# Performance work log

Hardware: AMD Instinct MI355X
Metric: run time of the kernel (lower is better)

The kernel has to match this reference:

```python
import jax, jax.numpy as jnp
import numpy as np

N_HEAD = 16
NEG = -1e9

def setup_inputs() -> dict:
    key = jax.random.key(0)
    k1, k2, k3 = jax.random.split(key, 3)
    B, S, NX = 8, 1024, 1024
    x = jax.random.normal(k1, (B, S, NX), dtype=jnp.float32)
    w_attn = jax.random.normal(k2, (NX, 3 * NX), dtype=jnp.float32) * 0.02
    b_attn = jnp.zeros((3 * NX,), dtype=jnp.float32)
    w_proj = jax.random.normal(k3, (NX, NX), dtype=jnp.float32) * 0.02
    b_proj = jnp.zeros((NX,), dtype=jnp.float32)
    return {"x": x, "w_attn": w_attn, "b_attn": b_attn, "w_proj": w_proj, "b_proj": b_proj}

def reference(x, w_attn, b_attn, w_proj, b_proj):
    B, S, NX = x.shape
    H = N_HEAD
    D = NX // H
    qkv = x @ w_attn + b_attn                      # [B,S,3*NX]
    q, k, v = jnp.split(qkv, 3, axis=-1)           # each [B,S,NX]
    q = q.reshape(B, S, H, D)
    k = k.reshape(B, S, H, D)
    v = v.reshape(B, S, H, D)
    # scores with scale (scale=True -> divide by sqrt(head_dim))
    w = jnp.einsum('bqhd,bkhd->bhqk', q, k) / jnp.sqrt(jnp.float32(D))
    tril = jnp.tril(jnp.ones((S, S), dtype=w.dtype))  # causal mask buffer
    w = w * tril + NEG * (1.0 - tril)
    w = jax.nn.softmax(w, axis=-1)                 # dropout is identity at eval
    a = jnp.einsum('bhqk,bkhd->bqhd', w, v)        # [B,S,H,D]
    a = a.reshape(B, S, NX)
    a = a @ w_proj + b_proj
    return a
```

## Files before the change

kernel.cpp:

```cpp
#include <hip/hip_runtime.h>
#include <hip/hip_bf16.h>
#include <stdint.h>

typedef __bf16 bf16x8 __attribute__((ext_vector_type(8)));
typedef float  f32x4  __attribute__((ext_vector_type(4)));
typedef float  f32x16 __attribute__((ext_vector_type(16)));

__device__ __forceinline__ void gload_lds16(const void* g, void* l) {
  __builtin_amdgcn_global_load_lds(
      (const __attribute__((address_space(1))) unsigned int*)g,
      (__attribute__((address_space(3))) unsigned int*)l, 16, 0, 0);
}

__global__ void k_cast(const float* __restrict__ in, __bf16* __restrict__ out, int n4) {
  int i = blockIdx.x * blockDim.x + threadIdx.x;
  if (i >= n4) return;
  float4 v = reinterpret_cast<const float4*>(in)[i];
  union { __bf16 h[4]; uint64_t u; } c;
  c.h[0] = (__bf16)v.x; c.h[1] = (__bf16)v.y; c.h[2] = (__bf16)v.z; c.h[3] = (__bf16)v.w;
  *reinterpret_cast<uint64_t*>(out + 4l * i) = c.u;
}

__global__ void k_transpose_cast(const float* __restrict__ in, __bf16* __restrict__ out,
                                 int R, int C) {
  __shared__ float t[32][33];
  const int tx = threadIdx.x & 31, ty = threadIdx.x >> 5;
  const int c0 = blockIdx.x * 32, r0 = blockIdx.y * 32;
#pragma unroll
  for (int rr = 0; rr < 4; ++rr)
    t[ty * 4 + rr][tx] = in[(long)(r0 + ty * 4 + rr) * C + c0 + tx];
  __syncthreads();
#pragma unroll
  for (int rr = 0; rr < 4; ++rr)
    out[(long)(c0 + ty * 4 + rr) * R + r0 + tx] = (__bf16)t[tx][ty * 4 + rr];
}

template <int MODE>
__global__ void k_gemm_bt(const __bf16* __restrict__ A, const __bf16* __restrict__ Bt,
                          const float* __restrict__ bias, int M, int N, int K,
                          __bf16* __restrict__ qo, __bf16* __restrict__ ko,
                          __bf16* __restrict__ vo, float* __restrict__ fo) {
  __shared__ __bf16 Ab[128 * 32];
  __shared__ __bf16 Bb[128 * 32];
  const int l = threadIdx.x & 63, w = threadIdx.x >> 6;
  const int wr = w >> 1, wc = w & 1;
  const int bm = blockIdx.y, bn = blockIdx.x;

  f32x4 acc[4][4] = {};

  const __bf16* Ag = A + (long)(bm * 128 + w * 32 + (l >> 2)) * K + (l & 3) * 8;
  const __bf16* Bg = Bt + (long)(bn * 128 + w * 32 + (l >> 2)) * K + (l & 3) * 8;
  char* Al = (char*)Ab + w * 2048;
  char* Bl = (char*)Bb + w * 2048;

  for (int k0 = 0; k0 < K; k0 += 32) {
    gload_lds16(Ag + k0, Al);
    gload_lds16(Ag + 16l * K + k0, Al + 1024);
    gload_lds16(Bg + k0, Bl);
    gload_lds16(Bg + 16l * K + k0, Bl + 1024);
    __syncthreads();

    bf16x8 af[4], bfr[4];
#pragma unroll
    for (int mi = 0; mi < 4; ++mi)
      af[mi] = *(const bf16x8*)&Ab[(wr * 64 + mi * 16 + (l & 15)) * 32 + ((l >> 4) << 3)];
#pragma unroll
    for (int ni = 0; ni < 4; ++ni)
      bfr[ni] = *(const bf16x8*)&Bb[(wc * 64 + ni * 16 + (l & 15)) * 32 + ((l >> 4) << 3)];
#pragma unroll
    for (int mi = 0; mi < 4; ++mi)
#pragma unroll
      for (int ni = 0; ni < 4; ++ni)
        acc[mi][ni] = __builtin_amdgcn_mfma_f32_16x16x32_bf16(af[mi], bfr[ni], acc[mi][ni], 0, 0, 0);
    __syncthreads();
  }

  if (MODE == 0) {
#pragma unroll
    for (int ni = 0; ni < 4; ++ni) {
      const int c = bn * 128 + wc * 64 + ni * 16 + (l & 15);
      const float bv = bias[c];
      const int which = c >> 10, cc = c & 1023, h = cc >> 6, d = cc & 63;
#pragma unroll
      for (int mi = 0; mi < 4; ++mi)
#pragma unroll
        for (int i = 0; i < 4; ++i) {
          const int r = bm * 128 + wr * 64 + mi * 16 + ((l >> 4) << 2) + i;
          const int b = r >> 10, s_ = r & 1023;
          float fv = acc[mi][ni][i] + bv;
          if (which == 0) fv *= 0.125f;
          const __bf16 v = (__bf16)fv;
          const long hb = (long)(b * 16 + h);
          if (which == 0)      qo[(hb * 1024 + s_) * 64 + d] = v;
          else if (which == 1) ko[(hb * 1024 + s_) * 64 + d] = v;
          else                 vo[(hb * 64 + d) * 1024 + s_] = v;
        }
    }
  } else {
#pragma unroll
    for (int ni = 0; ni < 4; ++ni) {
      const int c = bn * 128 + wc * 64 + ni * 16 + (l & 15);
      const float bv = bias[c];
#pragma unroll
      for (int mi = 0; mi < 4; ++mi)
#pragma unroll
        for (int i = 0; i < 4; ++i) {
          const int r = bm * 128 + wr * 64 + mi * 16 + ((l >> 4) << 2) + i;
          fo[(long)r * N + c] = acc[mi][ni][i] + bv;
        }
    }
  }
}

__device__ __forceinline__ void attn_qtile(const __bf16* __restrict__ Q,
                                           const __bf16* __restrict__ Kh,
                                           const __bf16* __restrict__ Vt,
                                           __bf16* __restrict__ ob,
                                           int b, int h, int qbw, int l) {
  const int lm = l & 31, hi = l >> 5;

  bf16x8 qf[4];
#pragma unroll
  for (int ds = 0; ds < 4; ++ds)
    qf[ds] = *(const bf16x8*)(Q + (long)(qbw + lm) * 64 + ds * 16 + hi * 8);

  f32x16 oacc0 = {}, oacc1 = {};
  float m = -__builtin_inff(), s = 0.f;

  const int ntiles = (qbw >> 5) + 1;
  for (int kt = 0; kt < ntiles; ++kt) {
    const int k0 = kt * 32;
    f32x16 st = {};
#pragma unroll
    for (int ds = 0; ds < 4; ++ds) {
      bf16x8 kf = *(const bf16x8*)(Kh + (long)(k0 + lm) * 64 + ds * 16 + hi * 8);
      st = __builtin_amdgcn_mfma_f32_32x32x16_bf16(kf, qf[ds], st, 0, 0, 0);
    }
    if (kt == ntiles - 1) {
      const int q = qbw + lm;
#pragma unroll
      for (int r = 0; r < 16; ++r) {
        const int key = k0 + (r & 3) + 8 * (r >> 2) + 4 * hi;
        if (key > q) st[r] = -__builtin_inff();
      }
    }
    float tm = st[0];
#pragma unroll
    for (int r = 1; r < 16; ++r) tm = fmaxf(tm, st[r]);
    tm = fmaxf(tm, __shfl_xor(tm, 32));
    if (!__all(tm <= m + 8.f)) {
      const float mn = fmaxf(m, tm);
      const float fac = __expf(m - mn);
      m = mn;
      s *= fac;
#pragma unroll
      for (int r = 0; r < 16; ++r) {
        const int qr = (r & 3) + 8 * (r >> 2) + 4 * hi;
        const float fr = __int_as_float(
            __builtin_amdgcn_ds_bpermute(qr * 4, __float_as_int(fac)));
        oacc0[r] *= fr; oacc1[r] *= fr;
      }
    }
    float p[16], ts = 0.f;
#pragma unroll
    for (int r = 0; r < 16; ++r) { p[r] = __expf(st[r] - m); ts += p[r]; }
    ts += __shfl_xor(ts, 32);
    s += ts;
    unsigned int w8[8];
#pragma unroll
    for (int t = 0; t < 8; ++t) {
      union { __bf16 hh[2]; unsigned int u; } pk;
      pk.hh[0] = (__bf16)p[2 * t]; pk.hh[1] = (__bf16)p[2 * t + 1];
      w8[t] = pk.u;
    }
    const unsigned int e0 = __shfl_xor(hi ? w8[0] : w8[2], 32);
    const unsigned int e1 = __shfl_xor(hi ? w8[1] : w8[3], 32);
    const unsigned int e2 = __shfl_xor(hi ? w8[4] : w8[6], 32);
    const unsigned int e3 = __shfl_xor(hi ? w8[5] : w8[7], 32);
    union { unsigned int wd[4]; bf16x8 v; } pa0, pa1;
    if (hi) {
      pa0.wd[0] = e0;    pa0.wd[1] = e1;    pa0.wd[2] = w8[2]; pa0.wd[3] = w8[3];
      pa1.wd[0] = e2;    pa1.wd[1] = e3;    pa1.wd[2] = w8[6]; pa1.wd[3] = w8[7];
    } else {
      pa0.wd[0] = w8[0]; pa0.wd[1] = w8[1]; pa0.wd[2] = e0;    pa0.wd[3] = e1;
      pa1.wd[0] = w8[4]; pa1.wd[1] = w8[5]; pa1.wd[2] = e2;    pa1.wd[3] = e3;
    }
#pragma unroll
    for (int t = 0; t < 2; ++t) {
      const bf16x8 pa = t ? pa1.v : pa0.v;
      bf16x8 vf0 = *(const bf16x8*)(Vt + (long)lm * 1024 + k0 + t * 16 + hi * 8);
      bf16x8 vf1 = *(const bf16x8*)(Vt + (long)(32 + lm) * 1024 + k0 + t * 16 + hi * 8);
      oacc0 = __builtin_amdgcn_mfma_f32_32x32x16_bf16(pa, vf0, oacc0, 0, 0, 0);
      oacc1 = __builtin_amdgcn_mfma_f32_32x32x16_bf16(pa, vf1, oacc1, 0, 0, 0);
    }
  }
  const float invs = 1.f / s;
#pragma unroll
  for (int r = 0; r < 16; ++r) {
    const int qr = (r & 3) + 8 * (r >> 2) + 4 * hi;
    const float inv = __int_as_float(
        __builtin_amdgcn_ds_bpermute(qr * 4, __float_as_int(invs)));
    const long row = (long)(b * 1024 + qbw + qr) * 1024 + h * 64;
    ob[row + lm]      = (__bf16)(oacc0[r] * inv);
    ob[row + 32 + lm] = (__bf16)(oacc1[r] * inv);
  }
}

__global__ void k_attn(const __bf16* __restrict__ qb_, const __bf16* __restrict__ kb,
                       const __bf16* __restrict__ vtb, __bf16* __restrict__ ob) {
  const int l = threadIdx.x & 63, w = threadIdx.x >> 6;
  const int bh = blockIdx.y, b = bh >> 4, h = bh & 15;
  const int wi = blockIdx.x * 4 + w;
  const __bf16* Q  = qb_ + (long)bh * 65536;
  const __bf16* Kh = kb  + (long)bh * 65536;
  const __bf16* Vt = vtb + (long)bh * 65536;
  attn_qtile(Q, Kh, Vt, ob, b, h, wi * 32, l);
  attn_qtile(Q, Kh, Vt, ob, b, h, (31 - wi) * 32, l);
}

extern "C" void kernel_launch(void* const* d_in, const int* in_sizes, int n_in,
                              void* d_out, int out_size, void* d_ws, size_t ws_size,
                              hipStream_t stream) {
  const float* x      = (const float*)d_in[0];
  const float* w_attn = (const float*)d_in[1];
  const float* b_attn = (const float*)d_in[2];
  const float* w_proj = (const float*)d_in[3];
  const float* b_proj = (const float*)d_in[4];
  float* out = (float*)d_out;

  char* ws = (char*)d_ws;
  const size_t SZ_XBF = (size_t)8192 * 1024 * 2;
  __bf16* x_bf = (__bf16*)ws;  ws += SZ_XBF;
  __bf16* wat  = (__bf16*)ws;  ws += (size_t)3072 * 1024 * 2;
  __bf16* wpt  = (__bf16*)ws;  ws += (size_t)1024 * 1024 * 2;
  __bf16* qb   = (__bf16*)ws;  ws += SZ_XBF;
  __bf16* kb   = (__bf16*)ws;  ws += SZ_XBF;
  __bf16* vtb  = (__bf16*)ws;  ws += SZ_XBF;
  __bf16* obf  = (__bf16*)ws;  ws += SZ_XBF;

  k_cast<<<8192, 256, 0, stream>>>(x, x_bf, 2097152);
  k_transpose_cast<<<dim3(96, 32), 256, 0, stream>>>(w_attn, wat, 1024, 3072);
  k_transpose_cast<<<dim3(32, 32), 256, 0, stream>>>(w_proj, wpt, 1024, 1024);
  k_gemm_bt<0><<<dim3(24, 64), 256, 0, stream>>>(x_bf, wat, b_attn, 8192, 3072, 1024,
                                                 qb, kb, vtb, nullptr);
  k_attn<<<dim3(4, 128), 256, 0, stream>>>(qb, kb, vtb, obf);
  k_gemm_bt<1><<<dim3(8, 64), 256, 0, stream>>>(obf, wpt, b_proj, 8192, 1024, 1024,
                                                nullptr, nullptr, nullptr, out);
}
```

Measured before the change: 286.9 us.

## Replace GEMM with double-buffered 256x128 pipelined kernel using swizzled LDS

New measurement: 279.0 us. 2.7% less time.

```diff
diff --git a/kernel.cpp b/kernel.cpp
--- a/kernel.cpp
+++ b/kernel.cpp
@@ -5,6 +5,9 @@
 typedef __bf16 bf16x8 __attribute__((ext_vector_type(8)));
 typedef float  f32x4  __attribute__((ext_vector_type(4)));
 typedef float  f32x16 __attribute__((ext_vector_type(16)));
+
+#define BARRIER() asm volatile("s_barrier" ::: "memory")
+#define VMCNT(n)  asm volatile("s_waitcnt vmcnt(" #n ")" ::: "memory")
 
 __device__ __forceinline__ void gload_lds16(const void* g, void* l) {
   __builtin_amdgcn_global_load_lds(
@@ -36,61 +39,129 @@
 }
 
 template <int MODE>
-__global__ void k_gemm_bt(const __bf16* __restrict__ A, const __bf16* __restrict__ Bt,
-                          const float* __restrict__ bias, int M, int N, int K,
-                          __bf16* __restrict__ qo, __bf16* __restrict__ ko,
-                          __bf16* __restrict__ vo, float* __restrict__ fo) {
-  __shared__ __bf16 Ab[128 * 32];
-  __shared__ __bf16 Bb[128 * 32];
-  const int l = threadIdx.x & 63, w = threadIdx.x >> 6;
-  const int wr = w >> 1, wc = w & 1;
-  const int bm = blockIdx.y, bn = blockIdx.x;
-
-  f32x4 acc[4][4] = {};
-
-  const __bf16* Ag = A + (long)(bm * 128 + w * 32 + (l >> 2)) * K + (l & 3) * 8;
-  const __bf16* Bg = Bt + (long)(bn * 128 + w * 32 + (l >> 2)) * K + (l & 3) * 8;
-  char* Al = (char*)Ab + w * 2048;
-  char* Bl = (char*)Bb + w * 2048;
-
-  for (int k0 = 0; k0 < K; k0 += 32) {
-    gload_lds16(Ag + k0, Al);
-    gload_lds16(Ag + 16l * K + k0, Al + 1024);
-    gload_lds16(Bg + k0, Bl);
-    gload_lds16(Bg + 16l * K + k0, Bl + 1024);
-    __syncthreads();
-
-    bf16x8 af[4], bfr[4];
-#pragma unroll
-    for (int mi = 0; mi < 4; ++mi)
-      af[mi] = *(const bf16x8*)&Ab[(wr * 64 + mi * 16 + (l & 15)) * 32 + ((l >> 4) << 3)];
-#pragma unroll
-    for (int ni = 0; ni < 4; ++ni)
-      bfr[ni] = *(const bf16x8*)&Bb[(wc * 64 + ni * 16 + (l & 15)) * 32 + ((l >> 4) << 3)];
-#pragma unroll
-    for (int mi = 0; mi < 4; ++mi)
-#pragma unroll
-      for (int ni = 0; ni < 4; ++ni)
-        acc[mi][ni] = __builtin_amdgcn_mfma_f32_16x16x32_bf16(af[mi], bfr[ni], acc[mi][ni], 0, 0, 0);
-    __syncthreads();
+__launch_bounds__(512, 2)
+__global__ void k_gemm_p(const __bf16* __restrict__ A, const __bf16* __restrict__ Bt,
+                         const float* __restrict__ bias, int M, int N, int K, int NB,
+                         __bf16* __restrict__ qo, __bf16* __restrict__ ko,
+                         __bf16* __restrict__ vo, float* __restrict__ fo) {
+  __shared__ __bf16 lds[2][3][8192];
+  const int tid = threadIdx.x;
+  const int l = tid & 63, w = tid >> 6;
+  const int lm = l & 15, lq = l >> 4;
+  const int wm = w >> 2, wn = w & 3;
+  const int nwg = gridDim.x;
+  const int wg = (blockIdx.x & 7) * (nwg >> 3) + (blockIdx.x >> 3);
+  const int bm = wg / NB, bn = wg % NB;
+  const int nt = K >> 6;
+
+  const int rh0 = tid >> 3;
+  const int scol = ((tid & 7) * 16) ^ ((rh0 & 7) << 4);
+  long a_off[2][2], b_off[2];
+#pragma unroll
+  for (int h = 0; h < 2; ++h)
+#pragma unroll
+    for (int li = 0; li < 2; ++li) {
+      const int row_h = li * 64 + rh0;
+      const int g_r = bm * 256 + ((row_h >> 4) << 5) + h * 16 + (row_h & 15);
+      a_off[h][li] = (long)g_r * K + (scol >> 1);
+    }
+#pragma unroll
+  for (int li = 0; li < 2; ++li)
+    b_off[li] = (long)(bn * 128 + li * 64 + rh0) * K + (scol >> 1);
+
+#define STAGE_AH(h, buf, t) { \
+    gload_lds16(A + a_off[h][0] + (long)(t) * 64, &lds[buf][h][tid * 8]); \
+    gload_lds16(A + a_off[h][1] + (long)(t) * 64, &lds[buf][h][4096 + tid * 8]); }
+#define STAGE_B(buf, t) { \
+    gload_lds16(Bt + b_off[0] + (long)(t) * 64, &lds[buf][2][tid * 8]); \
+    gload_lds16(Bt + b_off[1] + (long)(t) * 64, &lds[buf][2][4096 + tid * 8]); }
+
+  const int aswz = (lm & 7) << 4;
+
+  f32x4 acc[8][2] = {};
+
+  STAGE_B(0, 0); STAGE_AH(0, 0, 0); STAGE_AH(1, 0, 0);
+  VMCNT(2); BARRIER();
+
+  int cur = 0;
+  for (int t = 0; t < nt; ++t) {
+    const int nxt = cur ^ 1;
+    bf16x8 bf[2][2], ae[4][2];
+#pragma unroll
+    for (int nj = 0; nj < 2; ++nj)
+#pragma unroll
+      for (int ks = 0; ks < 2; ++ks) {
+        const int rh = wn * 32 + nj * 16 + lm;
+        bf[nj][ks] = *(const bf16x8*)&lds[cur][2][rh * 64 + (((ks * 64 + lq * 16) ^ aswz) >> 1)];
+      }
+#pragma unroll
+    for (int me = 0; me < 4; ++me)
+#pragma unroll
+      for (int ks = 0; ks < 2; ++ks) {
+        const int rh = (wm * 4 + me) * 16 + lm;
+        ae[me][ks] = *(const bf16x8*)&lds[cur][0][rh * 64 + (((ks * 64 + lq * 16) ^ aswz) >> 1)];
+      }
+    if (t + 1 < nt) {
+      STAGE_B(nxt, t + 1); STAGE_AH(0, nxt, t + 1);
+      VMCNT(4);
+    } else {
+      VMCNT(0);
+    }
+    BARRIER();
+    __builtin_amdgcn_s_setprio(1);
+#pragma unroll
+    for (int ks = 0; ks < 2; ++ks)
+#pragma unroll
+      for (int me = 0; me < 4; ++me)
+#pragma unroll
+        for (int nj = 0; nj < 2; ++nj)
+          acc[2 * me][nj] = __builtin_amdgcn_mfma_f32_16x16x32_bf16(ae[me][ks], bf[nj][ks],
+                                                                    acc[2 * me][nj], 0, 0, 0);
+    __builtin_amdgcn_s_setprio(0);
+    BARRIER();
+    bf16x8 ao[4][2];
+#pragma unroll
+    for (int mo = 0; mo < 4; ++mo)
+#pragma unroll
+      for (int ks = 0; ks < 2; ++ks) {
+        const int rh = (wm * 4 + mo) * 16 + lm;
+        ao[mo][ks] = *(const bf16x8*)&lds[cur][1][rh * 64 + (((ks * 64 + lq * 16) ^ aswz) >> 1)];
+      }
+    if (t + 1 < nt) {
+      STAGE_AH(1, nxt, t + 1);
+      VMCNT(2);
+    }
+    BARRIER();
+    __builtin_amdgcn_s_setprio(1);
+#pragma unroll
+    for (int ks = 0; ks < 2; ++ks)
+#pragma unroll
+      for (int mo = 0; mo < 4; ++mo)
+#pragma unroll
+        for (int nj = 0; nj < 2; ++nj)
+          acc[2 * mo + 1][nj] = __builtin_amdgcn_mfma_f32_16x16x32_bf16(ao[mo][ks], bf[nj][ks],
+                                                                        acc[2 * mo + 1][nj], 0, 0, 0);
+    __builtin_amdgcn_s_setprio(0);
+    BARRIER();
+    cur = nxt;
   }
 
   if (MODE == 0) {
 #pragma unroll
-    for (int ni = 0; ni < 4; ++ni) {
-      const int c = bn * 128 + wc * 64 + ni * 16 + (l & 15);
+    for (int nj = 0; nj < 2; ++nj) {
+      const int c = bn * 128 + wn * 32 + nj * 16 + lm;
       const float bv = bias[c];
-      const int which = c >> 10, cc = c & 1023, h = cc >> 6, d = cc & 63;
-#pragma unroll
-      for (int mi = 0; mi < 4; ++mi)
+      const int which = c >> 10, cc = c & 1023, hh = cc >> 6, d = cc & 63;
+#pragma unroll
+      for (int mi = 0; mi < 8; ++mi)
 #pragma unroll
         for (int i = 0; i < 4; ++i) {
-          const int r = bm * 128 + wr * 64 + mi * 16 + ((l >> 4) << 2) + i;
+          const int r = bm * 256 + wm * 128 + mi * 16 + lq * 4 + i;
           const int b = r >> 10, s_ = r & 1023;
-          float fv = acc[mi][ni][i] + bv;
+          float fv = acc[mi][nj][i] + bv;
           if (which == 0) fv *= 0.125f;
           const __bf16 v = (__bf16)fv;
-          const long hb = (long)(b * 16 + h);
+          const long hb = (long)(b * 16 + hh);
           if (which == 0)      qo[(hb * 1024 + s_) * 64 + d] = v;
           else if (which == 1) ko[(hb * 1024 + s_) * 64 + d] = v;
           else                 vo[(hb * 64 + d) * 1024 + s_] = v;
@@ -98,18 +169,20 @@
     }
   } else {
 #pragma unroll
-    for (int ni = 0; ni < 4; ++ni) {
-      const int c = bn * 128 + wc * 64 + ni * 16 + (l & 15);
+    for (int nj = 0; nj < 2; ++nj) {
+      const int c = bn * 128 + wn * 32 + nj * 16 + lm;
       const float bv = bias[c];
 #pragma unroll
-      for (int mi = 0; mi < 4; ++mi)
+      for (int mi = 0; mi < 8; ++mi)
 #pragma unroll
         for (int i = 0; i < 4; ++i) {
-          const int r = bm * 128 + wr * 64 + mi * 16 + ((l >> 4) << 2) + i;
-          fo[(long)r * N + c] = acc[mi][ni][i] + bv;
+          const int r = bm * 256 + wm * 128 + mi * 16 + lq * 4 + i;
+          fo[(long)r * N + c] = acc[mi][nj][i] + bv;
         }
     }
   }
+#undef STAGE_AH
+#undef STAGE_B
 }
 
 __device__ __forceinline__ void attn_qtile(const __bf16* __restrict__ Q,
@@ -241,9 +314,9 @@
   k_cast<<<8192, 256, 0, stream>>>(x, x_bf, 2097152);
   k_transpose_cast<<<dim3(96, 32), 256, 0, stream>>>(w_attn, wat, 1024, 3072);
   k_transpose_cast<<<dim3(32, 32), 256, 0, stream>>>(w_proj, wpt, 1024, 1024);
-  k_gemm_bt<0><<<dim3(24, 64), 256, 0, stream>>>(x_bf, wat, b_attn, 8192, 3072, 1024,
-                                                 qb, kb, vtb, nullptr);
+  k_gemm_p<0><<<768, 512, 0, stream>>>(x_bf, wat, b_attn, 8192, 3072, 1024, 24,
+                                       qb, kb, vtb, nullptr);
   k_attn<<<dim3(4, 128), 256, 0, stream>>>(qb, kb, vtb, obf);
-  k_gemm_bt<1><<<dim3(8, 64), 256, 0, stream>>>(obf, wpt, b_proj, 8192, 1024, 1024,
-                                                nullptr, nullptr, nullptr, out);
-}
+  k_gemm_p<1><<<256, 512, 0, stream>>>(obf, wpt, b_proj, 8192, 1024, 1024, 8,
+                                       nullptr, nullptr, nullptr, out);
+}
```
